# Performance work log

Measured on AMD Instinct MI355X. Metric: run time of the kernel, lower is better.

The kernel has to match this reference:

```python
import jax, jax.numpy as jnp
import numpy as np
import math

D_MODEL = 1024
H = 16
D_K = D_MODEL // H
SEQ = 4096
NEG = -1000000000.0  # mask constant from the original code


def setup_inputs() -> dict:
    key = jax.random.key(0)
    ks = jax.random.split(key, 7)
    return {
        "Q": jax.random.normal(ks[0], (SEQ, D_MODEL), dtype=jnp.float32),
        "K": jax.random.normal(ks[1], (SEQ, D_MODEL), dtype=jnp.float32),
        "V": jax.random.normal(ks[2], (SEQ, D_MODEL), dtype=jnp.float32),
        "W_Q": jax.random.normal(ks[3], (H, D_MODEL, D_K), dtype=jnp.float32),
        "W_K": jax.random.normal(ks[4], (H, D_MODEL, D_K), dtype=jnp.float32),
        "W_V": jax.random.normal(ks[5], (H, D_MODEL, D_K), dtype=jnp.float32),
        "W_O": jax.random.normal(ks[6], (D_MODEL, D_MODEL), dtype=jnp.float32),
        "mask": 1,
    }


def reference(Q, K, V, W_Q, W_K, W_V, W_O, mask):
    d_k = W_Q.shape[-1]
    s = Q.shape[0]
    # batched per-head projections: [h, s, d_k]
    Qh = jnp.einsum("sd,hdk->hsk", Q, W_Q)
    Kh = jnp.einsum("sd,hdk->hsk", K, W_K)
    Vh = jnp.einsum("sd,hdk->hsk", V, W_V)
    # scores: [h, s_q, s_k]
    scores = jnp.einsum("hqk,hsk->hqs", Qh, Kh) / math.sqrt(d_k)
    if mask:
        # faithful to torch: tril(scores) + triu(ones, 1) * -1e9
        lower = jnp.tril(jnp.ones((s, s), dtype=scores.dtype))
        upper = jnp.triu(jnp.ones((s, s), dtype=scores.dtype), k=1)
        scores = scores * lower + upper * NEG
    attn = jax.nn.softmax(scores, axis=-1)
    heads = jnp.einsum("hqs,hsk->hqk", attn, Vh)  # [h, s, d_k]
    # concat heads along feature dim in head order -> [s, h*d_k]
    concat = jnp.transpose(heads, (1, 0, 2)).reshape(s, -1)
    return concat @ W_O
```

## Files before the change

kernel.cpp:

```cpp
#include <hip/hip_runtime.h>
#include <hip/hip_bf16.h>

constexpr int S      = 4096;
constexpr int DMODEL = 1024;
constexpr int H      = 16;
constexpr int DK     = 64;

typedef __attribute__((ext_vector_type(8))) short          short8;
typedef __attribute__((ext_vector_type(4))) short          short4v;
typedef __attribute__((ext_vector_type(4))) float          float4v;
typedef __attribute__((ext_vector_type(4))) unsigned short ushort4v;
typedef __attribute__((ext_vector_type(8))) unsigned short ushort8;

__device__ __forceinline__ unsigned short f2bf(float x) {
    unsigned u = __builtin_bit_cast(unsigned, x);
    u += 0x7FFFu + ((u >> 16) & 1u);
    return (unsigned short)(u >> 16);
}
__device__ __forceinline__ float bf2f(unsigned short h) {
    unsigned u = ((unsigned)h) << 16;
    return __builtin_bit_cast(float, u);
}
__device__ __forceinline__ float fexp2(float x) { return __builtin_amdgcn_exp2f(x); }

__device__ __forceinline__ unsigned cvtpk_bf16(float lo, float hi) {
    unsigned r;
    asm("v_cvt_pk_bf16_f32 %0, %1, %2" : "=v"(r) : "v"(lo), "v"(hi));
    return r;
}

__device__ __forceinline__ void gl_lds16(const unsigned short* g, unsigned short* l) {
    __builtin_amdgcn_global_load_lds(
        (const __attribute__((address_space(1))) unsigned int*)g,
        (__attribute__((address_space(3))) unsigned int*)l, 16, 0, 0);
}

__global__ __launch_bounds__(256) void prep_all(
    const float* __restrict__ Q, const float* __restrict__ K,
    const float* __restrict__ V,
    const float* __restrict__ WQ, const float* __restrict__ WK,
    const float* __restrict__ WV, const float* __restrict__ WO,
    unsigned short* __restrict__ QH, unsigned short* __restrict__ QL,
    unsigned short* __restrict__ KH, unsigned short* __restrict__ KL,
    unsigned short* __restrict__ Vb,
    unsigned short* __restrict__ WqtH, unsigned short* __restrict__ WqtL,
    unsigned short* __restrict__ WktH, unsigned short* __restrict__ WktL,
    unsigned short* __restrict__ Wvt,  unsigned short* __restrict__ WOt)
{
    const int zb = blockIdx.z;
    const int t  = threadIdx.x;

    if (zb < 3) {
        const size_t base = ((size_t)blockIdx.x * 256 + t) * 8;
        const float* src = (zb == 0) ? Q : (zb == 1) ? K : V;
        const float4 a = *(const float4*)(src + base);
        const float4 b = *(const float4*)(src + base + 4);
        const float xs[8] = {a.x, a.y, a.z, a.w, b.x, b.y, b.z, b.w};
        ushort8 hv, lv;
#pragma unroll
        for (int j = 0; j < 8; ++j) {
            const unsigned short h = f2bf(xs[j]);
            hv[j] = h;
            lv[j] = f2bf(xs[j] - bf2f(h));
        }
        if (zb == 0)      { *(ushort8*)(QH + base) = hv; *(ushort8*)(QL + base) = lv; }
        else if (zb == 1) { *(ushort8*)(KH + base) = hv; *(ushort8*)(KL + base) = lv; }
        else              { *(ushort8*)(Vb + base) = hv; }
        return;
    }

    const int bb = blockIdx.x;
    if (bb >= 1024) return;
    const int zfull = bb >> 4;
    const int which = zfull >> 4;
    const int z     = zfull & 15;
    const int r0    = (bb & 15) * 64;

    __shared__ float Ts[64][65];

    const float* in;
    unsigned short *oh, *ol;
    int z_mult, rstride;
    if (which == 0)      { in = WQ; oh = WqtH; ol = WqtL; z_mult = 65536; rstride = 64; }
    else if (which == 1) { in = WK; oh = WktH; ol = WktL; z_mult = 65536; rstride = 64; }
    else if (which == 2) { in = WV; oh = Wvt;  ol = nullptr; z_mult = 65536; rstride = 64; }
    else                 { in = WO; oh = WOt;  ol = nullptr; z_mult = 64;    rstride = 1024; }

    const float* src = in + (size_t)z * z_mult;
#pragma unroll
    for (int i = 0; i < 4; ++i) {
        const int row = (t >> 4) + i * 16;
        const int col = (t & 15) * 4;
        const float4 v = *(const float4*)&src[(size_t)(r0 + row) * rstride + col];
        Ts[row][col + 0] = v.x; Ts[row][col + 1] = v.y;
        Ts[row][col + 2] = v.z; Ts[row][col + 3] = v.w;
    }
    __syncthreads();
#pragma unroll
    for (int i = 0; i < 4; ++i) {
        const int c  = (t >> 4) + i * 16;
        const int rb = (t & 15) * 4;
        ushort4v hv, lv;
#pragma unroll
        for (int j = 0; j < 4; ++j) {
            const float x = Ts[rb + j][c];
            const unsigned short h = f2bf(x);
            hv[j] = h;
            lv[j] = f2bf(x - bf2f(h));
        }
        const size_t o = (size_t)(z * 64 + c) * 1024 + r0 + rb;
        *(ushort4v*)&oh[o] = hv;
        if (ol) *(ushort4v*)&ol[o] = lv;
    }
}

template <bool SPLIT, int EPI>
__device__ __forceinline__ void gemm_core(unsigned short* __restrict__ sm,
                                          const unsigned short* __restrict__ Ah,
                                          const unsigned short* __restrict__ Al,
                                          const unsigned short* __restrict__ Bh,
                                          const unsigned short* __restrict__ Bl,
                                          float* __restrict__ C,
                                          unsigned short* __restrict__ O1,
                                          unsigned short* __restrict__ O2,
                                          int m0, int n0)
{
    unsigned short* AsH = sm;
    unsigned short* BsH = sm + 4096;
    unsigned short* AsL = sm + 8192;
    unsigned short* BsL = sm + 12288;

    const int t    = threadIdx.x;
    const int wave = t >> 6;
    const int lane = t & 63;
    const int quad = lane >> 4;
    const int l15  = lane & 15;
    const int wm   = (wave & 1) * 64;
    const int wn   = (wave >> 1) * 64;

    float4v acc[4][4];
#pragma unroll
    for (int mi = 0; mi < 4; ++mi)
#pragma unroll
        for (int ni = 0; ni < 4; ++ni)
#pragma unroll
            for (int r = 0; r < 4; ++r) acc[mi][ni][r] = 0.f;

    for (int k0 = 0; k0 < 1024; k0 += 32) {
        __syncthreads();
#pragma unroll
        for (int i = 0; i < 2; ++i) {
            const int c   = t + 256 * i;
            const int row = c >> 2;
            const int kc  = (c & 3) * 8;
            const int lb  = (i * 256 + wave * 64) * 8;
            gl_lds16(&Ah[(size_t)(m0 + row) * 1024 + k0 + kc], AsH + lb);
            gl_lds16(&Bh[(size_t)(n0 + row) * 1024 + k0 + kc], BsH + lb);
            if (SPLIT) {
                gl_lds16(&Al[(size_t)(m0 + row) * 1024 + k0 + kc], AsL + lb);
                gl_lds16(&Bl[(size_t)(n0 + row) * 1024 + k0 + kc], BsL + lb);
            }
        }
        __syncthreads();

        short8 afh[4], bfh[4], afl[4], bfl[4];
#pragma unroll
        for (int mi = 0; mi < 4; ++mi)
            afh[mi] = *(const short8*)&AsH[(wm + mi * 16 + l15) * 32 + quad * 8];
#pragma unroll
        for (int ni = 0; ni < 4; ++ni)
            bfh[ni] = *(const short8*)&BsH[(wn + ni * 16 + l15) * 32 + quad * 8];
        if (SPLIT) {
#pragma unroll
            for (int mi = 0; mi < 4; ++mi)
                afl[mi] = *(const short8*)&AsL[(wm + mi * 16 + l15) * 32 + quad * 8];
#pragma unroll
            for (int ni = 0; ni < 4; ++ni)
                bfl[ni] = *(const short8*)&BsL[(wn + ni * 16 + l15) * 32 + quad * 8];
        }

#pragma unroll
        for (int mi = 0; mi < 4; ++mi)
#pragma unroll
            for (int ni = 0; ni < 4; ++ni) {
                acc[mi][ni] = __builtin_amdgcn_mfma_f32_16x16x32_bf16(
                    afh[mi], bfh[ni], acc[mi][ni], 0, 0, 0);
                if (SPLIT) {
                    acc[mi][ni] = __builtin_amdgcn_mfma_f32_16x16x32_bf16(
                        afh[mi], bfl[ni], acc[mi][ni], 0, 0, 0);
                    acc[mi][ni] = __builtin_amdgcn_mfma_f32_16x16x32_bf16(
                        afl[mi], bfh[ni], acc[mi][ni], 0, 0, 0);
                }
            }
    }

    if (EPI == 2) {
        __syncthreads();
        unsigned short* Ts = sm;
#pragma unroll
        for (int mi = 0; mi < 4; ++mi)
#pragma unroll
            for (int ni = 0; ni < 4; ++ni) {
                ushort4v pk;
#pragma unroll
                for (int r = 0; r < 4; ++r) pk[r] = f2bf(acc[mi][ni][r]);
                *(ushort4v*)&Ts[(wn + ni * 16 + l15) * 136 + wm + mi * 16 + quad * 4] = pk;
            }
        __syncthreads();
#pragma unroll
        for (int p = 0; p < 8; ++p) {
            const int n = p * 16 + (t >> 4);
            const int m = (t & 15) * 8;
            *(ushort8*)&O1[(size_t)(n0 + n) * 4096 + m0 + m] =
                *(const ushort8*)&Ts[n * 136 + m];
        }
        return;
    }

#pragma unroll
    for (int mi = 0; mi < 4; ++mi)
#pragma unroll
        for (int r = 0; r < 4; ++r) {
            const int m = m0 + wm + mi * 16 + quad * 4 + r;
            if (EPI == 0) {
                float* cp = C + (size_t)m * 1024 + n0 + wn + l15;
#pragma unroll
                for (int ni = 0; ni < 4; ++ni) cp[ni * 16] = acc[mi][ni][r];
            } else {
                unsigned short* o1 = O1 + (size_t)m * 1024 + n0 + wn + l15;
                unsigned short* o2 = O2 + (size_t)m * 1024 + n0 + wn + l15;
#pragma unroll
                for (int ni = 0; ni < 4; ++ni) {
                    const float v = acc[mi][ni][r];
                    const unsigned short hh = f2bf(v);
                    o1[ni * 16] = hh;
                    o2[ni * 16] = f2bf(v - bf2f(hh));
                }
            }
        }
}

__global__ __launch_bounds__(256) void proj_mfma(
    const unsigned short* __restrict__ XqH, const unsigned short* __restrict__ XqL,
    const unsigned short* __restrict__ XkH, const unsigned short* __restrict__ XkL,
    const unsigned short* __restrict__ Xv,
    const unsigned short* __restrict__ WqtH, const unsigned short* __restrict__ WqtL,
    const unsigned short* __restrict__ WktH, const unsigned short* __restrict__ WktL,
    const unsigned short* __restrict__ Wvt,
    float* __restrict__ Qc,
    unsigned short* __restrict__ KHg, unsigned short* __restrict__ KLg,
    unsigned short* __restrict__ Vt)
{
    __shared__ __align__(16) unsigned short smem[17408];
    const int m0 = blockIdx.x * 128, n0 = blockIdx.y * 128;
    if (blockIdx.z == 0)
        gemm_core<true, 0>(smem, XqH, XqL, WqtH, WqtL, Qc, nullptr, nullptr, m0, n0);
    else if (blockIdx.z == 1)
        gemm_core<true, 1>(smem, XkH, XkL, WktH, WktL, nullptr, KHg, KLg, m0, n0);
    else
        gemm_core<false, 2>(smem, Xv, nullptr, Wvt, nullptr, nullptr, Vt, nullptr, m0, n0);
}

__global__ __launch_bounds__(256) void out_gemm_mfma(
    const unsigned short* __restrict__ Ocb,
    const unsigned short* __restrict__ WOt,
    float* __restrict__ out)
{
    __shared__ __align__(16) unsigned short smem[2 * 4096];
    gemm_core<false, 0>(smem, Ocb, nullptr, WOt, nullptr, out, nullptr, nullptr,
                        blockIdx.x * 128, blockIdx.y * 128);
}

__global__ __launch_bounds__(512) void attn_mfma(const float* __restrict__ Qc,
                                                 const unsigned short* __restrict__ KHg,
                                                 const unsigned short* __restrict__ KLg,
                                                 const unsigned short* __restrict__ Vtg,
                                                 unsigned short* __restrict__ Ocb)
{
    __shared__ __align__(16) short Khi[2][64][72];
    __shared__ __align__(16) short Klo[2][64][72];
    __shared__ __align__(16) short Vts[2][64][72];
    __shared__ __align__(16) short Pb[8][16][72];

    const int bid = blockIdx.x;
    const int h   = bid & 15;
    const int g   = bid >> 4;
    const int qb  = (g < 16) ? (31 - g) : (g - 16);
    const int q0  = qb * 128;
    const int nIt = qb + 1;

    const int t    = threadIdx.x;
    const int wave = t >> 6;
    const int lane = t & 63;
    const int quad = lane >> 4;
    const int l15  = lane & 15;

    constexpr float SCL = 0.18033688011112042f;

    short8 qhi[2], qlo[2];
    {
        const int qrow = q0 + wave * 16 + l15;
        const float* qp = Qc + (size_t)qrow * DMODEL + h * 64 + quad * 8;
#pragma unroll
        for (int ks = 0; ks < 2; ++ks) {
            float4 a = *(const float4*)(qp + ks * 32);
            float4 b = *(const float4*)(qp + ks * 32 + 4);
            const float xs[8] = {a.x, a.y, a.z, a.w, b.x, b.y, b.z, b.w};
#pragma unroll
            for (int j = 0; j < 8; ++j) {
                const unsigned short hi = f2bf(xs[j]);
                const unsigned short lo = f2bf(xs[j] - bf2f(hi));
                qhi[ks][j] = (short)hi;
                qlo[ks][j] = (short)lo;
            }
        }
    }

    short8 bones;
    {
        const short ob = (l15 == 0) ? (short)0x3F80 : (short)0;
#pragma unroll
        for (int j = 0; j < 8; ++j) bones[j] = ob;
    }

    float m_r[4] = {-1e30f, -1e30f, -1e30f, -1e30f};
    float4v lacc;
    float4v oacc[4];
#pragma unroll
    for (int r = 0; r < 4; ++r) lacc[r] = 0.f;
#pragma unroll
    for (int nt = 0; nt < 4; ++nt)
#pragma unroll
        for (int r = 0; r < 4; ++r) oacc[nt][r] = 0.f;

    const int srow = t >> 3;
    const int soff = (t & 7) * 8;

    ushort8 kh[2], kl[2], vt[2];
#pragma unroll
    for (int s = 0; s < 2; ++s) {
        const int krow = s * 64 + srow;
        kh[s] = *(const ushort8*)&KHg[(size_t)krow * 1024 + h * 64 + soff];
        kl[s] = *(const ushort8*)&KLg[(size_t)krow * 1024 + h * 64 + soff];
        vt[s] = *(const ushort8*)&Vtg[(size_t)(h * 64 + srow) * 4096 + s * 64 + soff];
    }

    const int qrow_lo = q0 + wave * 16;
    for (int it = 0; it < nIt; ++it) {
        const int jt0 = 2 * it;
#pragma unroll
        for (int s = 0; s < 2; ++s) {
            *(ushort8*)&Khi[s][srow][soff] = kh[s];
            *(ushort8*)&Klo[s][srow][soff] = kl[s];
            *(ushort8*)&Vts[s][srow][soff] = vt[s];
        }
        __syncthreads();

        if (it + 1 < nIt) {
#pragma unroll
            for (int s = 0; s < 2; ++s) {
                const int jn = (jt0 + 2 + s) * 64;
                kh[s] = *(const ushort8*)&KHg[(size_t)(jn + srow) * 1024 + h * 64 + soff];
                kl[s] = *(const ushort8*)&KLg[(size_t)(jn + srow) * 1024 + h * 64 + soff];
                vt[s] = *(const ushort8*)&Vtg[(size_t)(h * 64 + srow) * 4096 + jn + soff];
            }
        }

#pragma unroll
        for (int s = 0; s < 2; ++s) {
            const int j0 = (jt0 + s) * 64;
            if (j0 <= qrow_lo + 15) {
                float4v sacc[4];
#pragma unroll
                for (int nt = 0; nt < 4; ++nt)
#pragma unroll
                    for (int r = 0; r < 4; ++r) sacc[nt][r] = 0.f;
#pragma unroll
                for (int nt = 0; nt < 4; ++nt) {
                    const int key = nt * 16 + l15;
#pragma unroll
                    for (int ks = 0; ks < 2; ++ks) {
                        const short8 bh = *(const short8*)&Khi[s][key][ks * 32 + quad * 8];
                        const short8 bl = *(const short8*)&Klo[s][key][ks * 32 + quad * 8];
                        sacc[nt] = __builtin_amdgcn_mfma_f32_16x16x32_bf16(qhi[ks], bh, sacc[nt], 0, 0, 0);
                        sacc[nt] = __builtin_amdgcn_mfma_f32_16x16x32_bf16(qhi[ks], bl, sacc[nt], 0, 0, 0);
                        sacc[nt] = __builtin_amdgcn_mfma_f32_16x16x32_bf16(qlo[ks], bh, sacc[nt], 0, 0, 0);
                    }
                }

                if (j0 + 63 > qrow_lo) {
#pragma unroll
                    for (int nt = 0; nt < 4; ++nt) {
                        const int jg = j0 + nt * 16 + l15;
#pragma unroll
                        for (int r = 0; r < 4; ++r) {
                            const int qg = qrow_lo + quad * 4 + r;
                            if (jg > qg) sacc[nt][r] = -1e10f;
                        }
                    }
                }

                float rmax[4];
#pragma unroll
                for (int r = 0; r < 4; ++r)
                    rmax[r] = fmaxf(fmaxf(sacc[0][r], sacc[1][r]), fmaxf(sacc[2][r], sacc[3][r]));
#pragma unroll
                for (int off = 1; off < 16; off <<= 1)
#pragma unroll
                    for (int r = 0; r < 4; ++r)
                        rmax[r] = fmaxf(rmax[r], __shfl_xor(rmax[r], off));

                float rs[4];
#pragma unroll
                for (int r = 0; r < 4; ++r) rs[r] = rmax[r] * SCL;
                const bool grow = (rs[0] > m_r[0]) || (rs[1] > m_r[1]) ||
                                  (rs[2] > m_r[2]) || (rs[3] > m_r[3]);
                if (__any(grow)) {
#pragma unroll
                    for (int r = 0; r < 4; ++r) {
                        const float mn    = fmaxf(m_r[r], rs[r]);
                        const float alpha = fexp2(m_r[r] - mn);
                        m_r[r] = mn;
                        lacc[r] *= alpha;
#pragma unroll
                        for (int nt = 0; nt < 4; ++nt) oacc[nt][r] *= alpha;
                    }
                }

#pragma unroll
                for (int nt = 0; nt < 4; ++nt)
#pragma unroll
                    for (int r = 0; r < 4; ++r)
                        sacc[nt][r] = fexp2(__builtin_fmaf(sacc[nt][r], SCL, -m_r[r]));

#pragma unroll
                for (int r = 0; r < 4; ++r) {
                    const int prow = quad * 4 + r;
#pragma unroll
                    for (int np = 0; np < 2; ++np) {
                        const unsigned w = cvtpk_bf16(sacc[2 * np][r], sacc[2 * np + 1][r]);
                        Pb[wave][prow][(2 * np) * 16 + l15]     = (short)(w & 0xffffu);
                        Pb[wave][prow][(2 * np + 1) * 16 + l15] = (short)(w >> 16);
                    }
                }
                __asm__ volatile("s_waitcnt lgkmcnt(0)" ::: "memory");

                short8 af[2];
                af[0] = *(const short8*)&Pb[wave][l15][quad * 8];
                af[1] = *(const short8*)&Pb[wave][l15][32 + quad * 8];
#pragma unroll
                for (int nt = 0; nt < 4; ++nt) {
                    const int dk = nt * 16 + l15;
#pragma unroll
                    for (int ks = 0; ks < 2; ++ks) {
                        const short8 bv = *(const short8*)&Vts[s][dk][ks * 32 + quad * 8];
                        oacc[nt] = __builtin_amdgcn_mfma_f32_16x16x32_bf16(af[ks], bv, oacc[nt], 0, 0, 0);
                    }
                }
                lacc = __builtin_amdgcn_mfma_f32_16x16x32_bf16(af[0], bones, lacc, 0, 0, 0);
                lacc = __builtin_amdgcn_mfma_f32_16x16x32_bf16(af[1], bones, lacc, 0, 0, 0);
            }
        }
        __syncthreads();
    }

#pragma unroll
    for (int r = 0; r < 4; ++r) {
        const float lsum = __shfl(lacc[r], (lane & 48));
        const float inv  = 1.0f / lsum;
        const int qg = q0 + wave * 16 + quad * 4 + r;
        unsigned short* op = Ocb + (size_t)qg * DMODEL + h * 64 + l15;
#pragma unroll
        for (int nt = 0; nt < 4; ++nt)
            op[nt * 16] = f2bf(oacc[nt][r] * inv);
    }
}

extern "C" void kernel_launch(void* const* d_in, const int* in_sizes, int n_in,
                              void* d_out, int out_size, void* d_ws, size_t ws_size,
                              hipStream_t stream)
{
    const float* Q  = (const float*)d_in[0];
    const float* K  = (const float*)d_in[1];
    const float* V  = (const float*)d_in[2];
    const float* WQ = (const float*)d_in[3];
    const float* WK = (const float*)d_in[4];
    const float* WV = (const float*)d_in[5];
    const float* WO = (const float*)d_in[6];

    float* out = (float*)d_out;

    const size_t SD4 = (size_t)S * DMODEL * 4;
    const size_t SD2 = (size_t)S * DMODEL * 2;
    const size_t W2  = (size_t)DMODEL * DMODEL * 2;
    char* p = (char*)d_ws;
    auto take = [&](size_t b) { char* r = p; p += b; return r; };

    float* Qc = (float*)take(SD4);
    unsigned short* KHg = (unsigned short*)take(SD2);
    unsigned short* KLg = (unsigned short*)take(SD2);
    unsigned short* Vtg = (unsigned short*)take(SD2);
    unsigned short* XqH = (unsigned short*)take(SD2);
    unsigned short* XqL = (unsigned short*)take(SD2);
    unsigned short* XkH = (unsigned short*)take(SD2);
    unsigned short* XkL = (unsigned short*)take(SD2);
    unsigned short* Xv  = (unsigned short*)take(SD2);
    unsigned short* WqtH = (unsigned short*)take(W2);
    unsigned short* WqtL = (unsigned short*)take(W2);
    unsigned short* WktH = (unsigned short*)take(W2);
    unsigned short* WktL = (unsigned short*)take(W2);
    unsigned short* Wvt  = (unsigned short*)take(W2);
    unsigned short* WOt  = (unsigned short*)take(W2);
    unsigned short* Ocb  = (unsigned short*)take(SD2);

    prep_all<<<dim3(2048, 1, 4), 256, 0, stream>>>(
        Q, K, V, WQ, WK, WV, WO,
        XqH, XqL, XkH, XkL, Xv, WqtH, WqtL, WktH, WktL, Wvt, WOt);
    proj_mfma<<<dim3(S / 128, DMODEL / 128, 3), 256, 0, stream>>>(
        XqH, XqL, XkH, XkL, Xv, WqtH, WqtL, WktH, WktL, Wvt, Qc, KHg, KLg, Vtg);
    attn_mfma<<<dim3((S / 128) * H), 512, 0, stream>>>(Qc, KHg, KLg, Vtg, Ocb);
    out_gemm_mfma<<<dim3(S / 128, DMODEL / 128), 256, 0, stream>>>(Ocb, WOt, out);
}
```

Baseline: 328.9 us.

## Process two 16-row query fragments per wave in attention kernel with 256 threads

The attention kernel now uses 4 waves of 256 threads instead of 8 waves, with each wave handling 32 query rows as two 16-row fragments. Each K/V tile fragment read from LDS is reused across both fragments, halving the shared-memory reads per MFMA and leaving fewer waves to synchronise. In exchange each wave holds twice the accumulators and Q fragments, so register pressure rises and occupancy may fall. Global tile loads per thread also double.

```diff
diff --git a/kernel.cpp b/kernel.cpp
--- a/kernel.cpp
+++ b/kernel.cpp
@@ -271,7 +271,7 @@
                         blockIdx.x * 128, blockIdx.y * 128);
 }
 
-__global__ __launch_bounds__(512) void attn_mfma(const float* __restrict__ Qc,
+__global__ __launch_bounds__(256) void attn_mfma(const float* __restrict__ Qc,
                                                  const unsigned short* __restrict__ KHg,
                                                  const unsigned short* __restrict__ KLg,
                                                  const unsigned short* __restrict__ Vtg,
@@ -280,7 +280,7 @@
     __shared__ __align__(16) short Khi[2][64][72];
     __shared__ __align__(16) short Klo[2][64][72];
     __shared__ __align__(16) short Vts[2][64][72];
-    __shared__ __align__(16) short Pb[8][16][72];
+    __shared__ __align__(16) short Pb[4][2][16][72];
 
     const int bid = blockIdx.x;
     const int h   = bid & 15;
@@ -297,9 +297,10 @@
 
     constexpr float SCL = 0.18033688011112042f;
 
-    short8 qhi[2], qlo[2];
-    {
-        const int qrow = q0 + wave * 16 + l15;
+    short8 qhi[2][2], qlo[2][2];
+#pragma unroll
+    for (int f = 0; f < 2; ++f) {
+        const int qrow = q0 + wave * 32 + f * 16 + l15;
         const float* qp = Qc + (size_t)qrow * DMODEL + h * 64 + quad * 8;
 #pragma unroll
         for (int ks = 0; ks < 2; ++ks) {
@@ -310,8 +311,8 @@
             for (int j = 0; j < 8; ++j) {
                 const unsigned short hi = f2bf(xs[j]);
                 const unsigned short lo = f2bf(xs[j] - bf2f(hi));
-                qhi[ks][j] = (short)hi;
-                qlo[ks][j] = (short)lo;
+                qhi[f][ks][j] = (short)hi;
+                qlo[f][ks][j] = (short)lo;
             }
         }
     }
@@ -323,58 +324,73 @@
         for (int j = 0; j < 8; ++j) bones[j] = ob;
     }
 
-    float m_r[4] = {-1e30f, -1e30f, -1e30f, -1e30f};
-    float4v lacc;
-    float4v oacc[4];
-#pragma unroll
-    for (int r = 0; r < 4; ++r) lacc[r] = 0.f;
-#pragma unroll
-    for (int nt = 0; nt < 4; ++nt)
-#pragma unroll
-        for (int r = 0; r < 4; ++r) oacc[nt][r] = 0.f;
-
-    const int srow = t >> 3;
+    float m_r[2][4];
+    float4v lacc[2];
+    float4v oacc[2][4];
+#pragma unroll
+    for (int f = 0; f < 2; ++f) {
+#pragma unroll
+        for (int r = 0; r < 4; ++r) { m_r[f][r] = -1e30f; lacc[f][r] = 0.f; }
+#pragma unroll
+        for (int nt = 0; nt < 4; ++nt)
+#pragma unroll
+            for (int r = 0; r < 4; ++r) oacc[f][nt][r] = 0.f;
+    }
+
+    const int r0   = t >> 3;
     const int soff = (t & 7) * 8;
 
-    ushort8 kh[2], kl[2], vt[2];
-#pragma unroll
-    for (int s = 0; s < 2; ++s) {
-        const int krow = s * 64 + srow;
-        kh[s] = *(const ushort8*)&KHg[(size_t)krow * 1024 + h * 64 + soff];
-        kl[s] = *(const ushort8*)&KLg[(size_t)krow * 1024 + h * 64 + soff];
-        vt[s] = *(const ushort8*)&Vtg[(size_t)(h * 64 + srow) * 4096 + s * 64 + soff];
-    }
-
-    const int qrow_lo = q0 + wave * 16;
+    ushort8 kh[2][2], kl[2][2], vt[2][2];
+#pragma unroll
+    for (int s = 0; s < 2; ++s)
+#pragma unroll
+        for (int i = 0; i < 2; ++i) {
+            const int row = r0 + 32 * i;
+            kh[s][i] = *(const ushort8*)&KHg[(size_t)(s * 64 + row) * 1024 + h * 64 + soff];
+            kl[s][i] = *(const ushort8*)&KLg[(size_t)(s * 64 + row) * 1024 + h * 64 + soff];
+            vt[s][i] = *(const ushort8*)&Vtg[(size_t)(h * 64 + row) * 4096 + s * 64 + soff];
+        }
+
+    const int qw0 = q0 + wave * 32;
     for (int it = 0; it < nIt; ++it) {
         const int jt0 = 2 * it;
 #pragma unroll
-        for (int s = 0; s < 2; ++s) {
-            *(ushort8*)&Khi[s][srow][soff] = kh[s];
-            *(ushort8*)&Klo[s][srow][soff] = kl[s];
-            *(ushort8*)&Vts[s][srow][soff] = vt[s];
-        }
+        for (int s = 0; s < 2; ++s)
+#pragma unroll
+            for (int i = 0; i < 2; ++i) {
+                const int row = r0 + 32 * i;
+                *(ushort8*)&Khi[s][row][soff] = kh[s][i];
+                *(ushort8*)&Klo[s][row][soff] = kl[s][i];
+                *(ushort8*)&Vts[s][row][soff] = vt[s][i];
+            }
         __syncthreads();
 
         if (it + 1 < nIt) {
 #pragma unroll
-            for (int s = 0; s < 2; ++s) {
-                const int jn = (jt0 + 2 + s) * 64;
-                kh[s] = *(const ushort8*)&KHg[(size_t)(jn + srow) * 1024 + h * 64 + soff];
-                kl[s] = *(const ushort8*)&KLg[(size_t)(jn + srow) * 1024 + h * 64 + soff];
-                vt[s] = *(const ushort8*)&Vtg[(size_t)(h * 64 + srow) * 4096 + jn + soff];
-            }
+            for (int s = 0; s < 2; ++s)
+#pragma unroll
+                for (int i = 0; i < 2; ++i) {
+                    const int jn  = (jt0 + 2 + s) * 64;
+                    const int row = r0 + 32 * i;
+                    kh[s][i] = *(const ushort8*)&KHg[(size_t)(jn + row) * 1024 + h * 64 + soff];
+                    kl[s][i] = *(const ushort8*)&KLg[(size_t)(jn + row) * 1024 + h * 64 + soff];
+                    vt[s][i] = *(const ushort8*)&Vtg[(size_t)(h * 64 + row) * 4096 + jn + soff];
+                }
         }
 
 #pragma unroll
         for (int s = 0; s < 2; ++s) {
             const int j0 = (jt0 + s) * 64;
-            if (j0 <= qrow_lo + 15) {
-                float4v sacc[4];
-#pragma unroll
-                for (int nt = 0; nt < 4; ++nt)
-#pragma unroll
-                    for (int r = 0; r < 4; ++r) sacc[nt][r] = 0.f;
+            const bool act0 = (j0 <= qw0 + 15);
+            const bool act1 = (j0 <= qw0 + 31);
+            if (act1) {
+                float4v sacc[2][4];
+#pragma unroll
+                for (int f = 0; f < 2; ++f)
+#pragma unroll
+                    for (int nt = 0; nt < 4; ++nt)
+#pragma unroll
+                        for (int r = 0; r < 4; ++r) sacc[f][nt][r] = 0.f;
 #pragma unroll
                 for (int nt = 0; nt < 4; ++nt) {
                     const int key = nt * 16 + l15;
@@ -382,98 +398,122 @@
                     for (int ks = 0; ks < 2; ++ks) {
                         const short8 bh = *(const short8*)&Khi[s][key][ks * 32 + quad * 8];
                         const short8 bl = *(const short8*)&Klo[s][key][ks * 32 + quad * 8];
-                        sacc[nt] = __builtin_amdgcn_mfma_f32_16x16x32_bf16(qhi[ks], bh, sacc[nt], 0, 0, 0);
-                        sacc[nt] = __builtin_amdgcn_mfma_f32_16x16x32_bf16(qhi[ks], bl, sacc[nt], 0, 0, 0);
-                        sacc[nt] = __builtin_amdgcn_mfma_f32_16x16x32_bf16(qlo[ks], bh, sacc[nt], 0, 0, 0);
+                        if (act0) {
+                            sacc[0][nt] = __builtin_amdgcn_mfma_f32_16x16x32_bf16(qhi[0][ks], bh, sacc[0][nt], 0, 0, 0);
+                            sacc[0][nt] = __builtin_amdgcn_mfma_f32_16x16x32_bf16(qhi[0][ks], bl, sacc[0][nt], 0, 0, 0);
+                            sacc[0][nt] = __builtin_amdgcn_mfma_f32_16x16x32_bf16(qlo[0][ks], bh, sacc[0][nt], 0, 0, 0);
+                        }
+                        sacc[1][nt] = __builtin_amdgcn_mfma_f32_16x16x32_bf16(qhi[1][ks], bh, sacc[1][nt], 0, 0, 0);
+                        sacc[1][nt] = __builtin_amdgcn_mfma_f32_16x16x32_bf16(qhi[1][ks], bl, sacc[1][nt], 0, 0, 0);
+                        sacc[1][nt] = __builtin_amdgcn_mfma_f32_16x16x32_bf16(qlo[1][ks], bh, sacc[1][nt], 0, 0, 0);
                     }
                 }
 
-                if (j0 + 63 > qrow_lo) {
-#pragma unroll
-                    for (int nt = 0; nt < 4; ++nt) {
-                        const int jg = j0 + nt * 16 + l15;
-#pragma unroll
-                        for (int r = 0; r < 4; ++r) {
-                            const int qg = qrow_lo + quad * 4 + r;
-                            if (jg > qg) sacc[nt][r] = -1e10f;
+#pragma unroll
+                for (int f = 0; f < 2; ++f) {
+                    if (f == 0 && !act0) continue;
+                    const int qlo_f = qw0 + f * 16;
+
+                    if (j0 + 63 > qlo_f) {
+#pragma unroll
+                        for (int nt = 0; nt < 4; ++nt) {
+                            const int jg = j0 + nt * 16 + l15;
+#pragma unroll
+                            for (int r = 0; r < 4; ++r) {
+                                const int qg = qlo_f + quad * 4 + r;
+                                if (jg > qg) sacc[f][nt][r] = -1e10f;
+                            }
                         }
                     }
-                }
-
-                float rmax[4];
-#pragma unroll
-                for (int r = 0; r < 4; ++r)
-                    rmax[r] = fmaxf(fmaxf(sacc[0][r], sacc[1][r]), fmaxf(sacc[2][r], sacc[3][r]));
-#pragma unroll
-                for (int off = 1; off < 16; off <<= 1)
+
+                    float rmax[4];
 #pragma unroll
                     for (int r = 0; r < 4; ++r)
-                        rmax[r] = fmaxf(rmax[r], __shfl_xor(rmax[r], off));
-
-                float rs[4];
-#pragma unroll
-                for (int r = 0; r < 4; ++r) rs[r] = rmax[r] * SCL;
-                const bool grow = (rs[0] > m_r[0]) || (rs[1] > m_r[1]) ||
-                                  (rs[2] > m_r[2]) || (rs[3] > m_r[3]);
-                if (__any(grow)) {
+                        rmax[r] = fmaxf(fmaxf(sacc[f][0][r], sacc[f][1][r]),
+                                        fmaxf(sacc[f][2][r], sacc[f][3][r]));
+#pragma unroll
+                    for (int off = 1; off < 16; off <<= 1)
+#pragma unroll
+                        for (int r = 0; r < 4; ++r)
+                            rmax[r] = fmaxf(rmax[r], __shfl_xor(rmax[r], off));
+
+                    float rs[4];
+#pragma unroll
+                    for (int r = 0; r < 4; ++r) rs[r] = rmax[r] * SCL;
+                    const bool grow = (rs[0] > m_r[f][0]) || (rs[1] > m_r[f][1]) ||
+                                      (rs[2] > m_r[f][2]) || (rs[3] > m_r[f][3]);
+                    if (__any(grow)) {
+#pragma unroll
+                        for (int r = 0; r < 4; ++r) {
+                            const float mn    = fmaxf(m_r[f][r], rs[r]);
+                            const float alpha = fexp2(m_r[f][r] - mn);
+                            m_r[f][r] = mn;
+                            lacc[f][r] *= alpha;
+#pragma unroll
+                            for (int nt = 0; nt < 4; ++nt) oacc[f][nt][r] *= alpha;
+                        }
+                    }
+
+#pragma unroll
+                    for (int nt = 0; nt < 4; ++nt)
+#pragma unroll
+                        for (int r = 0; r < 4; ++r)
+                            sacc[f][nt][r] = fexp2(__builtin_fmaf(sacc[f][nt][r], SCL, -m_r[f][r]));
+
 #pragma unroll
                     for (int r = 0; r < 4; ++r) {
-                        const float mn    = fmaxf(m_r[r], rs[r]);
-                        const float alpha = fexp2(m_r[r] - mn);
-                        m_r[r] = mn;
-                        lacc[r] *= alpha;
-#pragma unroll
-                        for (int nt = 0; nt < 4; ++nt) oacc[nt][r] *= alpha;
+                        const int prow = quad * 4 + r;
+#pragma unroll
+                        for (int np = 0; np < 2; ++np) {
+                            const unsigned w = cvtpk_bf16(sacc[f][2 * np][r], sacc[f][2 * np + 1][r]);
+                            Pb[wave][f][prow][(2 * np) * 16 + l15]     = (short)(w & 0xffffu);
+                            Pb[wave][f][prow][(2 * np + 1) * 16 + l15] = (short)(w >> 16);
+                        }
                     }
                 }
-
-#pragma unroll
-                for (int nt = 0; nt < 4; ++nt)
-#pragma unroll
-                    for (int r = 0; r < 4; ++r)
-                        sacc[nt][r] = fexp2(__builtin_fmaf(sacc[nt][r], SCL, -m_r[r]));
-
-#pragma unroll
-                for (int r = 0; r < 4; ++r) {
-                    const int prow = quad * 4 + r;
-#pragma unroll
-                    for (int np = 0; np < 2; ++np) {
-                        const unsigned w = cvtpk_bf16(sacc[2 * np][r], sacc[2 * np + 1][r]);
-                        Pb[wave][prow][(2 * np) * 16 + l15]     = (short)(w & 0xffffu);
-                        Pb[wave][prow][(2 * np + 1) * 16 + l15] = (short)(w >> 16);
-                    }
-                }
                 __asm__ volatile("s_waitcnt lgkmcnt(0)" ::: "memory");
 
-                short8 af[2];
-                af[0] = *(const short8*)&Pb[wave][l15][quad * 8];
-                af[1] = *(const short8*)&Pb[wave][l15][32 + quad * 8];
+                short8 af0[2], af1[2];
+                if (act0) {
+                    af0[0] = *(const short8*)&Pb[wave][0][l15][quad * 8];
+                    af0[1] = *(const short8*)&Pb[wave][0][l15][32 + quad * 8];
+                }
+                af1[0] = *(const short8*)&Pb[wave][1][l15][quad * 8];
+                af1[1] = *(const short8*)&Pb[wave][1][l15][32 + quad * 8];
 #pragma unroll
                 for (int nt = 0; nt < 4; ++nt) {
                     const int dk = nt * 16 + l15;
 #pragma unroll
                     for (int ks = 0; ks < 2; ++ks) {
                         const short8 bv = *(const short8*)&Vts[s][dk][ks * 32 + quad * 8];
-                        oacc[nt] = __builtin_amdgcn_mfma_f32_16x16x32_bf16(af[ks], bv, oacc[nt], 0, 0, 0);
+                        if (act0)
+                            oacc[0][nt] = __builtin_amdgcn_mfma_f32_16x16x32_bf16(af0[ks], bv, oacc[0][nt], 0, 0, 0);
+                        oacc[1][nt] = __builtin_amdgcn_mfma_f32_16x16x32_bf16(af1[ks], bv, oacc[1][nt], 0, 0, 0);
                     }
                 }
-                lacc = __builtin_amdgcn_mfma_f32_16x16x32_bf16(af[0], bones, lacc, 0, 0, 0);
-                lacc = __builtin_amdgcn_mfma_f32_16x16x32_bf16(af[1], bones, lacc, 0, 0, 0);
+                if (act0) {
+                    lacc[0] = __builtin_amdgcn_mfma_f32_16x16x32_bf16(af0[0], bones, lacc[0], 0, 0, 0);
+                    lacc[0] = __builtin_amdgcn_mfma_f32_16x16x32_bf16(af0[1], bones, lacc[0], 0, 0, 0);
+                }
+                lacc[1] = __builtin_amdgcn_mfma_f32_16x16x32_bf16(af1[0], bones, lacc[1], 0, 0, 0);
+                lacc[1] = __builtin_amdgcn_mfma_f32_16x16x32_bf16(af1[1], bones, lacc[1], 0, 0, 0);
             }
         }
         __syncthreads();
     }
 
 #pragma unroll
-    for (int r = 0; r < 4; ++r) {
-        const float lsum = __shfl(lacc[r], (lane & 48));
-        const float inv  = 1.0f / lsum;
-        const int qg = q0 + wave * 16 + quad * 4 + r;
-        unsigned short* op = Ocb + (size_t)qg * DMODEL + h * 64 + l15;
-#pragma unroll
-        for (int nt = 0; nt < 4; ++nt)
-            op[nt * 16] = f2bf(oacc[nt][r] * inv);
-    }
+    for (int f = 0; f < 2; ++f)
+#pragma unroll
+        for (int r = 0; r < 4; ++r) {
+            const float lsum = __shfl(lacc[f][r], (lane & 48));
+            const float inv  = 1.0f / lsum;
+            const int qg = q0 + wave * 32 + f * 16 + quad * 4 + r;
+            unsigned short* op = Ocb + (size_t)qg * DMODEL + h * 64 + l15;
+#pragma unroll
+            for (int nt = 0; nt < 4; ++nt)
+                op[nt * 16] = f2bf(oacc[f][nt][r] * inv);
+        }
 }
 
 extern "C" void kernel_launch(void* const* d_in, const int* in_sizes, int n_in,
@@ -518,6 +558,6 @@
         XqH, XqL, XkH, XkL, Xv, WqtH, WqtL, WktH, WktL, Wvt, WOt);
     proj_mfma<<<dim3(S / 128, DMODEL / 128, 3), 256, 0, stream>>>(
         XqH, XqL, XkH, XkL, Xv, WqtH, WqtL, WktH, WktL, Wvt, Qc, KHg, KLg, Vtg);
-    attn_mfma<<<dim3((S / 128) * H), 512, 0, stream>>>(Qc, KHg, KLg, Vtg, Ocb);
+    attn_mfma<<<dim3((S / 128) * H), 256, 0, stream>>>(Qc, KHg, KLg, Vtg, Ocb);
     out_gemm_mfma<<<dim3(S / 128, DMODEL / 128), 256, 0, stream>>>(Ocb, WOt, out);
 }
```

New measurement: 449.1 us. 1.37x slower.

## Split long causal query blocks across two KV halves with combine kernel

Applied to the files above, without the earlier changes.

The attention grid goes from 32 to 48 work units per head. The 16 longest query blocks (rows 2048 and up) are each split into two KV-range pieces, and a lookup table orders the pieces so long work is scheduled first. Partial outputs, row maxima and row sums are written in fp32 to scratch space that reuses the XqH buffer, and a new combine kernel merges the two halves with log-sum-exp weights and writes bf16. The aim is to even out load across the causal triangle and reduce the tail where long blocks finish last. The cost is an extra kernel launch and extra global traffic for the partial results.

```diff
diff --git a/kernel.cpp b/kernel.cpp
--- a/kernel.cpp
+++ b/kernel.cpp
@@ -271,23 +271,46 @@
                         blockIdx.x * 128, blockIdx.y * 128);
 }
 
+__device__ const unsigned char PIECE[48] = {
+    31, 30, 63, 79,
+    29, 28, 62, 61, 78,
+    27, 26, 60, 59, 77,
+    25, 24, 58, 57, 76,
+    23, 22, 56, 55, 75,
+    21, 20, 54, 53, 74,
+    19, 18, 52, 51, 73,
+    17, 16, 50, 49, 72,
+    48, 71,
+    70, 69, 68, 67, 66, 65, 64
+};
+
 __global__ __launch_bounds__(512) void attn_mfma(const float* __restrict__ Qc,
                                                  const unsigned short* __restrict__ KHg,
                                                  const unsigned short* __restrict__ KLg,
                                                  const unsigned short* __restrict__ Vtg,
-                                                 unsigned short* __restrict__ Ocb)
+                                                 unsigned short* __restrict__ Ocb,
+                                                 float* __restrict__ Opart,
+                                                 float* __restrict__ Mp,
+                                                 float* __restrict__ Lp)
 {
     __shared__ __align__(16) short Khi[2][64][72];
     __shared__ __align__(16) short Klo[2][64][72];
     __shared__ __align__(16) short Vts[2][64][72];
     __shared__ __align__(16) short Pb[8][16][72];
 
-    const int bid = blockIdx.x;
-    const int h   = bid & 15;
-    const int g   = bid >> 4;
-    const int qb  = (g < 16) ? (31 - g) : (g - 16);
-    const int q0  = qb * 128;
-    const int nIt = qb + 1;
+    const int bid  = blockIdx.x;
+    const int u    = bid >> 4;
+    const int h    = bid & 15;
+    const int pc   = PIECE[u];
+    const int qb   = pc & 31;
+    const int kind = pc >> 5;
+    const int q0   = qb * 128;
+    const int nTot = qb + 1;
+    const int itA  = (qb + 2) >> 1;
+    const int it_lo = (kind == 1) ? itA : 0;
+    const int it_hi = (kind == 0) ? itA : nTot;
+    const bool partial = (kind < 2);
+    const int part = kind;
 
     const int t    = threadIdx.x;
     const int wave = t >> 6;
@@ -339,14 +362,14 @@
     ushort8 kh[2], kl[2], vt[2];
 #pragma unroll
     for (int s = 0; s < 2; ++s) {
-        const int krow = s * 64 + srow;
+        const int krow = (2 * it_lo + s) * 64 + srow;
         kh[s] = *(const ushort8*)&KHg[(size_t)krow * 1024 + h * 64 + soff];
         kl[s] = *(const ushort8*)&KLg[(size_t)krow * 1024 + h * 64 + soff];
-        vt[s] = *(const ushort8*)&Vtg[(size_t)(h * 64 + srow) * 4096 + s * 64 + soff];
+        vt[s] = *(const ushort8*)&Vtg[(size_t)(h * 64 + srow) * 4096 + (2 * it_lo + s) * 64 + soff];
     }
 
     const int qrow_lo = q0 + wave * 16;
-    for (int it = 0; it < nIt; ++it) {
+    for (int it = it_lo; it < it_hi; ++it) {
         const int jt0 = 2 * it;
 #pragma unroll
         for (int s = 0; s < 2; ++s) {
@@ -356,7 +379,7 @@
         }
         __syncthreads();
 
-        if (it + 1 < nIt) {
+        if (it + 1 < it_hi) {
 #pragma unroll
             for (int s = 0; s < 2; ++s) {
                 const int jn = (jt0 + 2 + s) * 64;
@@ -464,15 +487,67 @@
         __syncthreads();
     }
 
-#pragma unroll
-    for (int r = 0; r < 4; ++r) {
-        const float lsum = __shfl(lacc[r], (lane & 48));
-        const float inv  = 1.0f / lsum;
-        const int qg = q0 + wave * 16 + quad * 4 + r;
-        unsigned short* op = Ocb + (size_t)qg * DMODEL + h * 64 + l15;
-#pragma unroll
-        for (int nt = 0; nt < 4; ++nt)
-            op[nt * 16] = f2bf(oacc[nt][r] * inv);
+    if (!partial) {
+#pragma unroll
+        for (int r = 0; r < 4; ++r) {
+            const float lsum = __shfl(lacc[r], (lane & 48));
+            const float inv  = 1.0f / lsum;
+            const int qg = q0 + wave * 16 + quad * 4 + r;
+            unsigned short* op = Ocb + (size_t)qg * DMODEL + h * 64 + l15;
+#pragma unroll
+            for (int nt = 0; nt < 4; ++nt)
+                op[nt * 16] = f2bf(oacc[nt][r] * inv);
+        }
+    } else {
+        const size_t pstride = (size_t)16 * 2048;
+#pragma unroll
+        for (int r = 0; r < 4; ++r) {
+            const float lsum = __shfl(lacc[r], (lane & 48));
+            const int qg   = q0 + wave * 16 + quad * 4 + r;
+            const int qloc = qg - 2048;
+            const size_t ridx = (size_t)part * pstride + (size_t)h * 2048 + qloc;
+            float* op = Opart + ridx * 64 + l15;
+#pragma unroll
+            for (int nt = 0; nt < 4; ++nt)
+                op[nt * 16] = oacc[nt][r];
+            if (l15 == 0) { Mp[ridx] = m_r[r]; Lp[ridx] = lsum; }
+        }
+    }
+}
+
+__global__ __launch_bounds__(256) void combine_split(
+    const float* __restrict__ Opart,
+    const float* __restrict__ Mp,
+    const float* __restrict__ Lp,
+    unsigned short* __restrict__ Ocb)
+{
+    const int tid  = blockIdx.x * 256 + threadIdx.x;
+    const int row  = tid >> 2;
+    const int c0   = (tid & 3) * 16;
+    const int h    = row >> 11;
+    const int qloc = row & 2047;
+    const size_t pstride = (size_t)16 * 2048;
+    const size_t ridx = (size_t)h * 2048 + qloc;
+
+    const float mA = Mp[ridx], mB = Mp[pstride + ridx];
+    const float lA = Lp[ridx], lB = Lp[pstride + ridx];
+    const float m  = fmaxf(mA, mB);
+    const float wA = fexp2(mA - m), wB = fexp2(mB - m);
+    const float inv = 1.0f / (lA * wA + lB * wB);
+
+    const float* oA = Opart + ridx * 64 + c0;
+    const float* oB = Opart + (pstride + ridx) * 64 + c0;
+    unsigned short* out = Ocb + (size_t)(2048 + qloc) * DMODEL + h * 64 + c0;
+#pragma unroll
+    for (int j = 0; j < 16; j += 4) {
+        const float4 a = *(const float4*)(oA + j);
+        const float4 b = *(const float4*)(oB + j);
+        ushort4v o;
+        o[0] = f2bf((a.x * wA + b.x * wB) * inv);
+        o[1] = f2bf((a.y * wA + b.y * wB) * inv);
+        o[2] = f2bf((a.z * wA + b.z * wB) * inv);
+        o[3] = f2bf((a.w * wA + b.w * wB) * inv);
+        *(ushort4v*)(out + j) = o;
     }
 }
 
@@ -513,11 +588,17 @@
     unsigned short* WOt  = (unsigned short*)take(W2);
     unsigned short* Ocb  = (unsigned short*)take(SD2);
 
+    float* Opart = (float*)XqH;
+    float* Mp    = Opart + (size_t)2 * 16 * 2048 * 64;
+    float* Lp    = Mp    + (size_t)2 * 16 * 2048;
+
     prep_all<<<dim3(2048, 1, 4), 256, 0, stream>>>(
         Q, K, V, WQ, WK, WV, WO,
         XqH, XqL, XkH, XkL, Xv, WqtH, WqtL, WktH, WktL, Wvt, WOt);
     proj_mfma<<<dim3(S / 128, DMODEL / 128, 3), 256, 0, stream>>>(
         XqH, XqL, XkH, XkL, Xv, WqtH, WqtL, WktH, WktL, Wvt, Qc, KHg, KLg, Vtg);
-    attn_mfma<<<dim3((S / 128) * H), 512, 0, stream>>>(Qc, KHg, KLg, Vtg, Ocb);
+    attn_mfma<<<dim3(48 * H), 512, 0, stream>>>(Qc, KHg, KLg, Vtg, Ocb,
+                                                Opart, Mp, Lp);
+    combine_split<<<dim3(512), 256, 0, stream>>>(Opart, Mp, Lp, Ocb);
     out_gemm_mfma<<<dim3(S / 128, DMODEL / 128), 256, 0, stream>>>(Ocb, WOt, out);
 }
```

Measured after the change: 339.6 us. 1.03x slower.
